# Kernel tuning notes

Hardware: AMD Instinct MI355X
Metric: run time of the kernel (lower is better)

The kernel has to match this reference:

```python
import jax, jax.numpy as jnp
import numpy as np

RES = 0.03
NUM_ROTS = 36
NUM_PROPOSAL = 256
OVERSAMPLE = 4           # fixed-size stand-in for the data-dependent while loop
GX, GY, GZ = 272, 112, 272  # grid covering [-4,4.16] x [-0.2,3.16] x [-4,4.16] at res=0.03
POW = 0.5
SEED_DIST_THRESH = 0.3


def setup_inputs() -> dict:
    key = jax.random.key(0)
    ks = jax.random.split(key, 6)
    N, M = 100000, 1024
    extent = jnp.array([7.0, 3.0, 7.0], jnp.float32)
    offset = jnp.array([-3.5, 0.0, -3.5], jnp.float32)
    pc = jax.random.uniform(ks[0], (N, 3), jnp.float32) * extent + offset
    xyz = jax.random.uniform(ks[1], (N, 3), jnp.float32, minval=-0.3, maxval=0.3)
    scale = jax.random.uniform(ks[2], (N, 3), jnp.float32, minval=0.1, maxval=1.0)
    prob = jax.random.uniform(ks[3], (N,), jnp.float32)
    corners = jnp.array([[-4.0, -0.2, -4.0], [4.16, 3.16, 4.16]], jnp.float32)
    vote_points = jax.random.uniform(ks[4], (M, 3), jnp.float32) * extent + offset
    return dict(pc=pc, xyz=xyz, scale=scale, prob=prob, corners=corners, vote_points=vote_points)


def hough_vote(pc, xyz, scale, prob, corners):
    # Each point casts NUM_ROTS votes: center = pc + R_y(theta) @ xyz_offset
    thetas = 2.0 * jnp.pi * jnp.arange(NUM_ROTS, dtype=jnp.float32) / NUM_ROTS
    c, s = jnp.cos(thetas), jnp.sin(thetas)  # [R]
    ox, oy, oz = xyz[:, 0:1], xyz[:, 1:2], xyz[:, 2:3]  # [N,1]
    rx = ox * c + oz * s      # [N,R]
    rz = -ox * s + oz * c     # [N,R]
    tx = pc[:, 0:1] + rx
    ty = jnp.broadcast_to(pc[:, 1:2] + oy, tx.shape)
    tz = pc[:, 2:3] + rz
    ix = jnp.floor((tx - corners[0, 0]) / RES + 0.5).astype(jnp.int32)
    iy = jnp.floor((ty - corners[0, 1]) / RES + 0.5).astype(jnp.int32)
    iz = jnp.floor((tz - corners[0, 2]) / RES + 0.5).astype(jnp.int32)
    inb = ((ix >= 0) & (ix < GX) & (iy >= 0) & (iy < GY) & (iz >= 0) & (iz < GZ))
    ixc = jnp.clip(ix, 0, GX - 1)
    iyc = jnp.clip(iy, 0, GY - 1)
    izc = jnp.clip(iz, 0, GZ - 1)
    flat = ((ixc * GY + iyc) * GZ + izc).ravel()  # [N*R]
    w = (prob[:, None] * inb.astype(prob.dtype))  # [N,R]
    grid_obj = jnp.zeros((GX * GY * GZ,), pc.dtype).at[flat].add(w.ravel())
    ws = (w[:, :, None] * scale[:, None, :]).reshape(-1, 3)
    grid_scale = jnp.zeros((GX * GY * GZ, 3), pc.dtype).at[flat].add(ws)
    hv_map = grid_obj.reshape(GX, GY, GZ)
    hv_scale = (grid_scale / (grid_obj[:, None] + 1e-7)).reshape(GX, GY, GZ, 3)
    return hv_map, hv_scale


def reference(pc, xyz, scale, prob, corners, vote_points):
    hv_map, hv_scale = hough_vote(pc, xyz, scale, prob, corners)
    hv_map_y = jnp.power(hv_map.max(axis=1) + 1e-7, POW)  # [GX,GZ]
    hv_map_yidx = jnp.argmax(hv_map, axis=1)              # [GX,GZ]
    dist = hv_map_y.reshape(-1)
    finite = jnp.isfinite(dist)
    safe = jnp.where(finite, dist, 0.0)
    ok = finite.all() & (safe.sum() >= 1e-7)
    dist = jnp.where(ok, safe, 1.0)

    # fixed-size oversampling instead of the data-dependent while loop
    K = NUM_PROPOSAL * OVERSAMPLE
    sample = jax.random.categorical(jax.random.key(42), jnp.log(dist + 1e-30), shape=(K,))
    sample_val = dist[sample]
    xi = sample // GZ
    zi = sample % GZ
    yi = hv_map_yidx[xi, zi]
    world_loc = jnp.stack([xi, yi, zi], -1).astype(pc.dtype) * RES + corners[0]  # [K,3]
    sc = hv_scale[xi, yi, zi, :]  # [K,3]

    # min distance to vote seeds; keep candidates near seeds (fallback: keep all)
    d2seed = jnp.min(jnp.linalg.norm(world_loc[:, None, :] - vote_points[None, :, :], axis=-1), axis=-1)
    keep = d2seed < SEED_DIST_THRESH
    keep = jnp.where(keep.any(), keep, jnp.ones_like(keep))
    order = jnp.argsort(jnp.where(keep, 0, 1))  # stable: passing candidates first
    sel = order[:NUM_PROPOSAL]
    candidates = world_loc[sel]
    scales_out = sc[sel]
    probs = jnp.zeros((NUM_PROPOSAL,), pc.dtype)
    return candidates, probs, scales_out
```

## Files before the change

### kernel.cpp

```cpp
#include <hip/hip_runtime.h>
#include <math.h>
#include <stdio.h>
#include <stdint.h>

#define GXD 272
#define GYD 112
#define GZD 272
#define NROT 36
#define CCLS (GXD*GZD)
#define KSMP 1024
#define NPROP 256
#define HSLOTS 2048
#define YH 56
#define NBINS (GXD*2)
#define SLICE (GYD*GZD)
#define SVCAP 64
#define ROWG 16

struct RotTab { float c[NROT]; float s[NROT]; };

__device__ __forceinline__ uint32_t cell_hash(int flat) {
    return ((uint32_t)flat * 2654435761u) >> 21;
}

#define ROTL_AB(x, r) __builtin_amdgcn_alignbit((x), (x), 32u - (r))

__device__ __forceinline__ void threefry2x32(uint32_t k0, uint32_t k1,
                                             uint32_t x0, uint32_t x1,
                                             uint32_t& o0, uint32_t& o1) {
    uint32_t ks2 = k0 ^ k1 ^ 0x1BD11BDAu;
#define TF_ROUND(r) { x0 += x1; x1 = ROTL_AB(x1, r); x1 ^= x0; }
    x0 += k0; x1 += k1;
    TF_ROUND(13) TF_ROUND(15) TF_ROUND(26) TF_ROUND(6)
    x0 += k1;  x1 += ks2 + 1u;
    TF_ROUND(17) TF_ROUND(29) TF_ROUND(16) TF_ROUND(24)
    x0 += ks2; x1 += k0 + 2u;
    TF_ROUND(13) TF_ROUND(15) TF_ROUND(26) TF_ROUND(6)
    x0 += k0;  x1 += k1 + 3u;
    TF_ROUND(17) TF_ROUND(29) TF_ROUND(16) TF_ROUND(24)
    x0 += k1;  x1 += ks2 + 4u;
    TF_ROUND(13) TF_ROUND(15) TF_ROUND(26) TF_ROUND(6)
    x0 += ks2; x1 += k0 + 5u;
#undef TF_ROUND
    o0 = x0; o1 = x1;
}

__device__ __forceinline__ uint32_t tf_bits(uint32_t i) {
    uint32_t o0, o1;
    threefry2x32(0u, 42u, 0u, i, o0, o1);
    return o0 ^ o1;
}

__device__ __forceinline__ float uniform_from_bits(uint32_t b) {
    const float TINY = 1.1754943508222875e-38f;
    float f = __uint_as_float((b >> 9) | 0x3f800000u) - 1.0f;
    float u = __fadd_rn(__fmul_rn(f, 1.0f), TINY);
    return fmaxf(TINY, u);
}

__device__ __forceinline__ float gumbel_from_u(float u) {
    float l1 = (float)log((double)u);
    float l2 = (float)log((double)(-l1));
    return -l2;
}

__device__ __forceinline__ bool vote_iy(float py, float oy, float c0y, int& iy) {
    float ty = __fadd_rn(py, oy);
    float vy = __fadd_rn(__fdiv_rn(__fsub_rn(ty, c0y), 0.03f), 0.5f);
    iy = (int)floorf(vy);
    return (iy >= 0 && iy < GYD);
}
__device__ __forceinline__ bool vote_xz(float px, float pz, float ox, float oz,
                                        float c, float s, float c0x, float c0z,
                                        int& ix, int& iz) {
    float rx = __fadd_rn(__fmul_rn(ox, c), __fmul_rn(oz, s));
    float rz = __fadd_rn(__fmul_rn(-ox, s), __fmul_rn(oz, c));
    float tx = __fadd_rn(px, rx);
    float tz = __fadd_rn(pz, rz);
    float vx = __fadd_rn(__fdiv_rn(__fsub_rn(tx, c0x), 0.03f), 0.5f);
    float vz = __fadd_rn(__fdiv_rn(__fsub_rn(tz, c0z), 0.03f), 0.5f);
    ix = (int)floorf(vx);
    iz = (int)floorf(vz);
    return (ix >= 0 && ix < GXD && iz >= 0 && iz < GZD);
}
__device__ __forceinline__ bool vote_cell(float px, float py, float pz,
                                          float ox, float oy, float oz,
                                          float c, float s,
                                          float c0x, float c0y, float c0z,
                                          int& flat) {
    int iy, ix, iz;
    if (!vote_iy(py, oy, c0y, iy)) return false;
    if (!vote_xz(px, pz, ox, oz, c, s, c0x, c0z, ix, iz)) return false;
    flat = (ix*GYD + iy)*GZD + iz;
    return true;
}

__global__ __launch_bounds__(256) void k_count(const float* __restrict__ pc, const float* __restrict__ xyz,
                          const float* __restrict__ corners, int N, RotTab rt,
                          int* __restrict__ bincnt) {
    __shared__ int h[NBINS];
    int tid = threadIdx.x;
    for (int j = tid; j < NBINS; j += 256) h[j] = 0;
    __syncthreads();
    int i = blockIdx.x * 256 + tid;
    if (i < N) {
        float px = pc[3*i], py = pc[3*i+1], pz = pc[3*i+2];
        float ox = xyz[3*i], oy = xyz[3*i+1], oz = xyz[3*i+2];
        int iy;
        if (vote_iy(py, oy, corners[1], iy)) {
            int ybit = (iy >= YH) ? 1 : 0;
            float c0x = corners[0], c0z = corners[2];
            for (int r = 0; r < NROT; ++r) {
                int ix, iz;
                if (vote_xz(px, pz, ox, oz, rt.c[r], rt.s[r], c0x, c0z, ix, iz))
                    atomicAdd(&h[ix*2 + ybit], 1);
            }
        }
    }
    __syncthreads();
    for (int j = tid; j < NBINS; j += 256) if (h[j]) atomicAdd(&bincnt[j], h[j]);
}

__global__ __launch_bounds__(576) void k_prefix(const int* __restrict__ bincnt,
                         int* __restrict__ binbase, int* __restrict__ bincur) {
    __shared__ int sc[576];
    int tid = threadIdx.x;
    int v = (tid < NBINS) ? bincnt[tid] : 0;
    sc[tid] = v;
    __syncthreads();
    for (int off = 1; off < 576; off <<= 1) {
        int x = sc[tid];
        if (tid >= off) x += sc[tid - off];
        __syncthreads();
        sc[tid] = x;
        __syncthreads();
    }
    if (tid < NBINS) {
        int excl = sc[tid] - v;
        binbase[tid] = excl;
        bincur[tid] = excl;
    }
}

__global__ __launch_bounds__(256) void k_binwrite(const float* __restrict__ pc, const float* __restrict__ xyz,
                          const float* __restrict__ prob, const float* __restrict__ corners,
                          int N, RotTab rt, int* __restrict__ bincur,
                          int* __restrict__ vflat, float* __restrict__ vw) {
    __shared__ int h[NBINS];
    __shared__ int bbase[NBINS];
    int tid = threadIdx.x;
    for (int j = tid; j < NBINS; j += 256) h[j] = 0;
    __syncthreads();
    int i = blockIdx.x * 256 + tid;
    float px=0, py=0, pz=0, ox=0, oy=0, oz=0, w0=0, c0x=0, c0z=0;
    int iy = -1, ybit = 0;
    bool act = false;
    if (i < N) {
        px = pc[3*i]; py = pc[3*i+1]; pz = pc[3*i+2];
        ox = xyz[3*i]; oy = xyz[3*i+1]; oz = xyz[3*i+2];
        w0 = prob[i];
        c0x = corners[0]; c0z = corners[2];
        if (vote_iy(py, oy, corners[1], iy)) {
            act = true;
            ybit = (iy >= YH) ? 1 : 0;
        }
    }
    if (act) {
        for (int r = 0; r < NROT; ++r) {
            int ix, iz;
            if (vote_xz(px, pz, ox, oz, rt.c[r], rt.s[r], c0x, c0z, ix, iz))
                atomicAdd(&h[ix*2 + ybit], 1);
        }
    }
    __syncthreads();
    for (int j = tid; j < NBINS; j += 256) {
        int cnt = h[j];
        bbase[j] = cnt ? atomicAdd(&bincur[j], cnt) : 0;
        h[j] = 0;
    }
    __syncthreads();
    if (act) {
        for (int r = 0; r < NROT; ++r) {
            int ix, iz;
            if (vote_xz(px, pz, ox, oz, rt.c[r], rt.s[r], c0x, c0z, ix, iz)) {
                int bin = ix*2 + ybit;
                int rank = atomicAdd(&h[bin], 1);
                int slot = bbase[bin] + rank;
                vflat[slot] = (ix*GYD + iy)*GZD + iz;
                vw[slot] = w0;
            }
        }
    }
}

__global__ __launch_bounds__(256) void k_accum(const int* __restrict__ binbase,
                          const int* __restrict__ bincnt,
                          const int* __restrict__ vflat, const float* __restrict__ vw,
                          float* __restrict__ gobj) {
    __shared__ float tile[YH*GZD];
    int b = blockIdx.x;
    int x = b >> 1, yh = b & 1;
    int tid = threadIdx.x;
    for (int j = tid; j < YH*GZD; j += 256) tile[j] = 0.0f;
    __syncthreads();
    int lo = binbase[b], n = bincnt[b];
    int xoff = x * SLICE;
    int yoff = yh * (YH*GZD);
    for (int j = lo + tid; j < lo + n; j += 256) {
        int rel = vflat[j] - xoff;
        atomicAdd(&tile[rel - yoff], vw[j]);
    }
    __syncthreads();
    float* dst = gobj + (size_t)xoff + yoff;
    for (int j = tid; j < YH*GZD; j += 256) dst[j] = tile[j];
}

__global__ __launch_bounds__(256) void k_colmax(const float* __restrict__ gobj,
                         float* __restrict__ logits, int* __restrict__ yidx,
                         float* __restrict__ sumdist) {
    int c = blockIdx.x * blockDim.x + threadIdx.x;
    float d = 0.0f;
    if (c < CCLS) {
        int x = c / GZD, z = c % GZD;
        const float* base = gobj + (size_t)x*GYD*GZD + z;
        float m = base[0];
        int mi = 0;
        for (int y = 1; y < GYD; ++y) {
            float v = base[(size_t)y*GZD];
            if (v > m) { m = v; mi = y; }
        }
        d = __fsqrt_rn(__fadd_rn(m, 1e-7f));
        yidx[c] = mi;
        logits[c] = (float)log((double)__fadd_rn(d, 1e-30f));
    }
    __shared__ float sred[256];
    int tid = threadIdx.x;
    sred[tid] = d; __syncthreads();
    for (int off = 128; off > 0; off >>= 1) {
        if (tid < off) sred[tid] += sred[tid+off];
        __syncthreads();
    }
    if (tid == 0) atomicAdd(sumdist, sred[0]);
}

__global__ __launch_bounds__(256) void k_thresh(const float* __restrict__ logits,
                                                const float* __restrict__ sumdist,
                                                uint32_t* __restrict__ bth) {
    int c = blockIdx.x * blockDim.x + threadIdx.x;
    if (c >= CCLS) return;
    double B0 = log((double)*sumdist) - 3.0;
    double t = exp(-exp((double)logits[c] - (B0 - 0.05)));
    long long k_th = (long long)floor(t * 8388608.0) - 2;
    uint32_t b;
    if (k_th <= 0)              b = 0u;
    else if (k_th >= 8388608LL) b = 0xFFFFFFFFu;
    else                        b = (uint32_t)k_th << 9;
    bth[c] = b;
}

__global__ __launch_bounds__(256) void k_prefilter(const uint32_t* __restrict__ bth,
                                                   int* __restrict__ svcnt,
                                                   uint2* __restrict__ svrec) {
    int c = blockIdx.x * 256 + threadIdx.x;
    int k0 = blockIdx.y * (KSMP / ROWG);
    uint32_t th = bth[c];
    uint32_t i = (uint32_t)k0 * (uint32_t)CCLS + (uint32_t)c;
#pragma unroll 4
    for (int kk = 0; kk < KSMP / ROWG; ++kk) {
        uint32_t bits = tf_bits(i);
        if (__builtin_expect(bits >= th, 0)) {
            int row = k0 + kk;
            int idx = atomicAdd(&svcnt[row], 1);
            if (idx < SVCAP) svrec[row * SVCAP + idx] = make_uint2((uint32_t)c, bits);
        }
        i += (uint32_t)CCLS;
    }
}

__global__ __launch_bounds__(256) void k_finalize(const float* __restrict__ logits,
                                                  const int* __restrict__ svcnt,
                                                  const uint2* __restrict__ svrec,
                                                  int* __restrict__ samples) {
    int k = blockIdx.x;
    int tid = threadIdx.x;
    int n = svcnt[k];
    float best = -INFINITY; int bc = 0x7fffffff;
    if (n > 0 && n <= SVCAP) {
        if (tid < n) {
            uint2 rec = svrec[k * SVCAP + tid];
            int c = (int)rec.x;
            best = __fadd_rn(gumbel_from_u(uniform_from_bits(rec.y)), logits[c]);
            bc = c;
        }
    } else {
        uint32_t base = (uint32_t)k * (uint32_t)CCLS;
        for (int c = tid; c < CCLS; c += 256) {
            float v = __fadd_rn(gumbel_from_u(uniform_from_bits(tf_bits(base + (uint32_t)c))), logits[c]);
            if (v > best || (v == best && c < bc)) { best = v; bc = c; }
        }
    }
    __shared__ float sv[256];
    __shared__ int   si[256];
    sv[tid] = best; si[tid] = bc; __syncthreads();
    for (int off = 128; off > 0; off >>= 1) {
        if (tid < off) {
            float v2 = sv[tid+off]; int i2 = si[tid+off];
            if (v2 > sv[tid] || (v2 == sv[tid] && i2 < si[tid])) { sv[tid] = v2; si[tid] = i2; }
        }
        __syncthreads();
    }
    if (tid == 0) samples[k] = si[0];
}

__global__ __launch_bounds__(256) void k_build_table(const int* __restrict__ samples,
                                                     const int* __restrict__ yidx,
                                                     int* __restrict__ hkeys,
                                                     float* __restrict__ gsmall) {
    int tid = threadIdx.x;
    for (int j = tid; j < HSLOTS; j += 256) hkeys[j] = -1;
    for (int j = tid; j < 3*HSLOTS; j += 256) gsmall[j] = 0.0f;
    __syncthreads();
    for (int k = tid; k < KSMP; k += 256) {
        int s = samples[k];
        int xi = s / GZD, zi = s % GZD;
        int yi = yidx[s];
        int flat = (xi*GYD + yi)*GZD + zi;
        uint32_t h = cell_hash(flat);
        for (;;) {
            int prev = atomicCAS(&hkeys[h], -1, flat);
            if (prev == -1 || prev == flat) break;
            h = (h + 1) & (HSLOTS - 1);
        }
    }
}

__global__ __launch_bounds__(256) void k_scale_scatter(const float* __restrict__ pc, const float* __restrict__ xyz,
                          const float* __restrict__ scale, const float* __restrict__ prob,
                          const float* __restrict__ corners,
                          const int* __restrict__ hkeys, float* __restrict__ gsmall,
                          int N, RotTab rt) {
    __shared__ int lk[HSLOTS];
    for (int j = threadIdx.x; j < HSLOTS; j += 256) lk[j] = hkeys[j];
    __syncthreads();
    int i = blockIdx.x * blockDim.x + threadIdx.x;
    int r = blockIdx.y;
    if (i >= N) return;
    int flat;
    if (!vote_cell(pc[3*i], pc[3*i+1], pc[3*i+2], xyz[3*i], xyz[3*i+1], xyz[3*i+2],
                   rt.c[r], rt.s[r], corners[0], corners[1], corners[2], flat)) return;
    uint32_t h = cell_hash(flat);
    int slot = -1;
    for (;;) {
        int key = lk[h];
        if (key == flat) { slot = (int)h; break; }
        if (key == -1) break;
        h = (h + 1) & (HSLOTS - 1);
    }
    if (slot < 0) return;
    float w0 = prob[i];
    atomicAdd(&gsmall[3*slot+0], __fmul_rn(w0, scale[3*i]));
    atomicAdd(&gsmall[3*slot+1], __fmul_rn(w0, scale[3*i+1]));
    atomicAdd(&gsmall[3*slot+2], __fmul_rn(w0, scale[3*i+2]));
}

__global__ __launch_bounds__(256) void k_post(const float* __restrict__ gobj,
                       const int* __restrict__ hkeys, const float* __restrict__ gsmall,
                       const int* __restrict__ yidx, const int* __restrict__ samples,
                       const float* __restrict__ corners, const float* __restrict__ vp, int M,
                       float* __restrict__ world, float* __restrict__ scv, int* __restrict__ keep) {
    int k = blockIdx.x;
    int tid = threadIdx.x;
    int s = samples[k];
    int xi = s / GZD, zi = s % GZD;
    int yi = yidx[s];
    float wx = __fadd_rn(__fmul_rn((float)xi, 0.03f), corners[0]);
    float wy = __fadd_rn(__fmul_rn((float)yi, 0.03f), corners[1]);
    float wz = __fadd_rn(__fmul_rn((float)zi, 0.03f), corners[2]);

    float dmin = INFINITY;
    for (int j = tid; j < M; j += 256) {
        float dx = __fsub_rn(wx, vp[3*j]);
        float dy = __fsub_rn(wy, vp[3*j+1]);
        float dz = __fsub_rn(wz, vp[3*j+2]);
        float sq = __fadd_rn(__fadd_rn(__fmul_rn(dx,dx), __fmul_rn(dy,dy)), __fmul_rn(dz,dz));
        dmin = fminf(dmin, __fsqrt_rn(sq));
    }
    __shared__ float sm[256];
    sm[tid] = dmin; __syncthreads();
    for (int off = 128; off > 0; off >>= 1) {
        if (tid < off) sm[tid] = fminf(sm[tid], sm[tid+off]);
        __syncthreads();
    }
    if (tid == 0) {
        world[3*k] = wx; world[3*k+1] = wy; world[3*k+2] = wz;
        int flat = (xi*GYD + yi)*GZD + zi;
        uint32_t h = cell_hash(flat);
        while (hkeys[h] != flat) h = (h + 1) & (HSLOTS - 1);
        float go = __fadd_rn(gobj[flat], 1e-7f);
        scv[3*k+0] = __fdiv_rn(gsmall[3*h+0], go);
        scv[3*k+1] = __fdiv_rn(gsmall[3*h+1], go);
        scv[3*k+2] = __fdiv_rn(gsmall[3*h+2], go);
        keep[k] = (sm[0] < 0.3f) ? 1 : 0;
    }
}

__global__ __launch_bounds__(256) void k_select(const float* __restrict__ world,
                                                const float* __restrict__ scv,
                                                const int* __restrict__ keep,
                                                float* __restrict__ out) {
    __shared__ int kp[KSMP];
    __shared__ int tsum[256];
    __shared__ int sel[NPROP];
    __shared__ int anyk;
    int tid = threadIdx.x;
    if (tid == 0) anyk = 0;
    __syncthreads();
    int a = 0;
    for (int j = tid; j < KSMP; j += 256) { int v = keep[j]; kp[j] = v; a |= v; }
    if (a) anyk = 1;
    __syncthreads();
    int any = anyk;
    int j0 = tid * 4;
    int k0v = any ? kp[j0]   : 1;
    int k1v = any ? kp[j0+1] : 1;
    int k2v = any ? kp[j0+2] : 1;
    int k3v = any ? kp[j0+3] : 1;
    int s0 = k0v, s1 = s0 + k1v, s2 = s1 + k2v, s3 = s2 + k3v;
    tsum[tid] = s3;
    __syncthreads();
    for (int off = 1; off < 256; off <<= 1) {
        int x = tsum[tid];
        if (tid >= off) x += tsum[tid - off];
        __syncthreads();
        tsum[tid] = x;
        __syncthreads();
    }
    int base = (tid > 0) ? tsum[tid-1] : 0;
    int nk = tsum[255];
    int inc[4] = { base + s0, base + s1, base + s2, base + s3 };
    int kv[4]  = { k0v, k1v, k2v, k3v };
    for (int q = 0; q < 4; ++q) {
        int j = j0 + q;
        int slot = kv[q] ? (inc[q] - 1) : (nk + j - inc[q]);
        if (slot < NPROP) sel[slot] = j;
    }
    __syncthreads();
    if (tid < NPROP) {
        int sidx = sel[tid];
        out[3*tid+0] = world[3*sidx+0];
        out[3*tid+1] = world[3*sidx+1];
        out[3*tid+2] = world[3*sidx+2];
        out[3*NPROP + tid] = 0.0f;
        out[4*NPROP + 3*tid + 0] = scv[3*sidx+0];
        out[4*NPROP + 3*tid + 1] = scv[3*sidx+1];
        out[4*NPROP + 3*tid + 2] = scv[3*sidx+2];
    }
}

extern "C" void kernel_launch(void* const* d_in, const int* in_sizes, int n_in,
                              void* d_out, int out_size, void* d_ws, size_t ws_size,
                              hipStream_t stream) {
    const float* pc      = (const float*)d_in[0];
    const float* xyz     = (const float*)d_in[1];
    const float* scale   = (const float*)d_in[2];
    const float* prob    = (const float*)d_in[3];
    const float* corners = (const float*)d_in[4];
    const float* vp      = (const float*)d_in[5];
    int N = in_sizes[0] / 3;
    int M = in_sizes[5] / 3;
    int NV = N * NROT;

    const size_t G = (size_t)GXD * GYD * GZD;
    float* gobj    = (float*)d_ws;
    float* sumdist = gobj + G;
    int*   bincnt  = (int*)(sumdist + 1);
    int*   svcnt   = bincnt + NBINS;
    int*   binbase = svcnt + KSMP;
    int*   bincur  = binbase + NBINS;
    float* logits  = (float*)(bincur + NBINS);
    uint32_t* bth  = (uint32_t*)(logits + CCLS);
    int*   yidx    = (int*)(bth + CCLS);
    int*   samples = yidx + CCLS;
    int*   hkeys   = samples + KSMP;
    float* gsmall  = (float*)(hkeys + HSLOTS);
    float* world   = gsmall + 3*HSLOTS;
    float* scv     = world + 3*KSMP;
    int*   keep    = (int*)(scv + 3*KSMP);
    uint2* svrec   = (uint2*)(((uintptr_t)(keep + KSMP) + 15) & ~(uintptr_t)15);
    int*   vflat   = (int*)(svrec + (size_t)KSMP * SVCAP);
    float* vw      = (float*)(vflat + NV);
    size_t need = (size_t)((char*)(vw + NV) - (char*)d_ws);
    if (ws_size < need) {
        fprintf(stderr, "kernel_launch: ws_size %zu < needed %zu\n", ws_size, need);
        return;
    }

    hipMemsetAsync(sumdist, 0, (1 + NBINS + KSMP)*sizeof(int), stream);

    RotTab rt;
    const float twopi = (float)(2.0 * M_PI);
    for (int r = 0; r < NROT; ++r) {
        float th = (twopi * (float)r) / 36.0f;
        rt.c[r] = (float)cos((double)th);
        rt.s[r] = (float)sin((double)th);
    }

    int pblocks = (N + 255) / 256;
    k_count<<<pblocks, 256, 0, stream>>>(pc, xyz, corners, N, rt, bincnt);
    k_prefix<<<1, 576, 0, stream>>>(bincnt, binbase, bincur);
    k_binwrite<<<pblocks, 256, 0, stream>>>(pc, xyz, prob, corners, N, rt, bincur, vflat, vw);
    k_accum<<<NBINS, 256, 0, stream>>>(binbase, bincnt, vflat, vw, gobj);
    k_colmax<<<(CCLS + 255) / 256, 256, 0, stream>>>(gobj, logits, yidx, sumdist);
    k_thresh<<<(CCLS + 255) / 256, 256, 0, stream>>>(logits, sumdist, bth);
    dim3 pf_grid(CCLS / 256, ROWG);
    k_prefilter<<<pf_grid, 256, 0, stream>>>(bth, svcnt, svrec);
    k_finalize<<<KSMP, 256, 0, stream>>>(logits, svcnt, svrec, samples);
    k_build_table<<<1, 256, 0, stream>>>(samples, yidx, hkeys, gsmall);
    dim3 sgrid(pblocks, NROT);
    k_scale_scatter<<<sgrid, 256, 0, stream>>>(pc, xyz, scale, prob, corners, hkeys, gsmall, N, rt);
    k_post<<<KSMP, 256, 0, stream>>>(gobj, hkeys, gsmall, yidx, samples, corners, vp, M, world, scv, keep);
    k_select<<<1, 256, 0, stream>>>(world, scv, keep, (float*)d_out);
}
```

Baseline: 422.7 us.

## Replace count+prefix passes with per-block segment arena binning; loop rotations in scale scatter

Removes the separate counting and global prefix kernels. Each binwrite block now reserves one contiguous arena range with a single atomic and records a per-bin segment (start, count). The accumulate kernel rebuilds each bin's element list by scanning its segments and binary-searching the prefix. The scale scatter kernel now loops over the 36 rotations inside each thread instead of using a 2D grid, so per-point loads and the y test are done once. The costs are extra scan and binary-search work in accumulate, scattered segment reads, and a hard cap of 512 blocks per bin.

```diff
diff --git a/kernel.cpp b/kernel.cpp
--- a/kernel.cpp
+++ b/kernel.cpp
@@ -16,6 +16,7 @@
 #define SLICE (GYD*GZD)
 #define SVCAP 64
 #define ROWG 16
+#define MAXSEG 512
 
 struct RotTab { float c[NROT]; float s[NROT]; };
 
@@ -83,74 +84,21 @@
     iz = (int)floorf(vz);
     return (ix >= 0 && ix < GXD && iz >= 0 && iz < GZD);
 }
-__device__ __forceinline__ bool vote_cell(float px, float py, float pz,
-                                          float ox, float oy, float oz,
-                                          float c, float s,
-                                          float c0x, float c0y, float c0z,
-                                          int& flat) {
-    int iy, ix, iz;
-    if (!vote_iy(py, oy, c0y, iy)) return false;
-    if (!vote_xz(px, pz, ox, oz, c, s, c0x, c0z, ix, iz)) return false;
-    flat = (ix*GYD + iy)*GZD + iz;
-    return true;
-}
-
-__global__ __launch_bounds__(256) void k_count(const float* __restrict__ pc, const float* __restrict__ xyz,
-                          const float* __restrict__ corners, int N, RotTab rt,
-                          int* __restrict__ bincnt) {
-    __shared__ int h[NBINS];
-    int tid = threadIdx.x;
-    for (int j = tid; j < NBINS; j += 256) h[j] = 0;
-    __syncthreads();
-    int i = blockIdx.x * 256 + tid;
-    if (i < N) {
-        float px = pc[3*i], py = pc[3*i+1], pz = pc[3*i+2];
-        float ox = xyz[3*i], oy = xyz[3*i+1], oz = xyz[3*i+2];
-        int iy;
-        if (vote_iy(py, oy, corners[1], iy)) {
-            int ybit = (iy >= YH) ? 1 : 0;
-            float c0x = corners[0], c0z = corners[2];
-            for (int r = 0; r < NROT; ++r) {
-                int ix, iz;
-                if (vote_xz(px, pz, ox, oz, rt.c[r], rt.s[r], c0x, c0z, ix, iz))
-                    atomicAdd(&h[ix*2 + ybit], 1);
-            }
-        }
-    }
-    __syncthreads();
-    for (int j = tid; j < NBINS; j += 256) if (h[j]) atomicAdd(&bincnt[j], h[j]);
-}
-
-__global__ __launch_bounds__(576) void k_prefix(const int* __restrict__ bincnt,
-                         int* __restrict__ binbase, int* __restrict__ bincur) {
-    __shared__ int sc[576];
-    int tid = threadIdx.x;
-    int v = (tid < NBINS) ? bincnt[tid] : 0;
-    sc[tid] = v;
-    __syncthreads();
-    for (int off = 1; off < 576; off <<= 1) {
-        int x = sc[tid];
-        if (tid >= off) x += sc[tid - off];
-        __syncthreads();
-        sc[tid] = x;
-        __syncthreads();
-    }
-    if (tid < NBINS) {
-        int excl = sc[tid] - v;
-        binbase[tid] = excl;
-        bincur[tid] = excl;
-    }
-}
 
 __global__ __launch_bounds__(256) void k_binwrite(const float* __restrict__ pc, const float* __restrict__ xyz,
                           const float* __restrict__ prob, const float* __restrict__ corners,
-                          int N, RotTab rt, int* __restrict__ bincur,
+                          int N, RotTab rt,
+                          int* __restrict__ arena_cur, int* __restrict__ segcnt,
+                          int2* __restrict__ segrec,
                           int* __restrict__ vflat, float* __restrict__ vw) {
     __shared__ int h[NBINS];
-    __shared__ int bbase[NBINS];
+    __shared__ int loff[NBINS];
+    __shared__ int tsum[256];
+    __shared__ int sbase;
     int tid = threadIdx.x;
     for (int j = tid; j < NBINS; j += 256) h[j] = 0;
     __syncthreads();
+
     int i = blockIdx.x * 256 + tid;
     float px=0, py=0, pz=0, ox=0, oy=0, oz=0, w0=0, c0x=0, c0z=0;
     int iy = -1, ybit = 0;
@@ -173,19 +121,45 @@
         }
     }
     __syncthreads();
+
+    int c0 = h[tid];
+    int c1 = h[tid + 256];
+    int c2 = (tid < NBINS - 512) ? h[tid + 512] : 0;
+    tsum[tid] = c0 + c1 + c2;
+    __syncthreads();
+    for (int off = 1; off < 256; off <<= 1) {
+        int v = tsum[tid];
+        if (tid >= off) v += tsum[tid - off];
+        __syncthreads();
+        tsum[tid] = v;
+        __syncthreads();
+    }
+    int base = (tid > 0) ? tsum[tid-1] : 0;
+    int total = tsum[255];
+    if (tid == 0) sbase = total ? atomicAdd(arena_cur, total) : 0;
+    loff[tid] = base;
+    loff[tid + 256] = base + c0;
+    if (tid < NBINS - 512) loff[tid + 512] = base + c0 + c1;
+    __syncthreads();
+    int gb = sbase;
+
     for (int j = tid; j < NBINS; j += 256) {
         int cnt = h[j];
-        bbase[j] = cnt ? atomicAdd(&bincur[j], cnt) : 0;
+        if (cnt) {
+            int idx = atomicAdd(&segcnt[j], 1);
+            if (idx < MAXSEG) segrec[j*MAXSEG + idx] = make_int2(gb + loff[j], cnt);
+        }
         h[j] = 0;
     }
     __syncthreads();
+
     if (act) {
         for (int r = 0; r < NROT; ++r) {
             int ix, iz;
             if (vote_xz(px, pz, ox, oz, rt.c[r], rt.s[r], c0x, c0z, ix, iz)) {
                 int bin = ix*2 + ybit;
                 int rank = atomicAdd(&h[bin], 1);
-                int slot = bbase[bin] + rank;
+                int slot = gb + loff[bin] + rank;
                 vflat[slot] = (ix*GYD + iy)*GZD + iz;
                 vw[slot] = w0;
             }
@@ -193,22 +167,50 @@
     }
 }
 
-__global__ __launch_bounds__(256) void k_accum(const int* __restrict__ binbase,
-                          const int* __restrict__ bincnt,
+__global__ __launch_bounds__(256) void k_accum(const int* __restrict__ segcnt,
+                          const int2* __restrict__ segrec,
                           const int* __restrict__ vflat, const float* __restrict__ vw,
                           float* __restrict__ gobj) {
     __shared__ float tile[YH*GZD];
+    __shared__ int sstart[512];
+    __shared__ int spre[513];
     int b = blockIdx.x;
     int x = b >> 1, yh = b & 1;
     int tid = threadIdx.x;
     for (int j = tid; j < YH*GZD; j += 256) tile[j] = 0.0f;
-    __syncthreads();
-    int lo = binbase[b], n = bincnt[b];
+    int ns = segcnt[b];
+    int a0 = 0, a1 = 0, st0 = 0, st1 = 0;
+    if (tid < ns)       { int2 r = segrec[b*MAXSEG + tid];       st0 = r.x; a0 = r.y; }
+    if (tid + 256 < ns) { int2 r = segrec[b*MAXSEG + tid + 256]; st1 = r.x; a1 = r.y; }
+    sstart[tid] = a0 + a1;
+    __syncthreads();
+    for (int off = 1; off < 256; off <<= 1) {
+        int v = sstart[tid];
+        if (tid >= off) v += sstart[tid - off];
+        __syncthreads();
+        sstart[tid] = v;
+        __syncthreads();
+    }
+    int base = (tid > 0) ? sstart[tid-1] : 0;
+    int total = sstart[255];
+    __syncthreads();
+    spre[2*tid]   = base;
+    spre[2*tid+1] = base + a0;
+    sstart[2*tid]   = st0;
+    sstart[2*tid+1] = st1;
+    if (tid == 0) spre[512] = total;
+    __syncthreads();
     int xoff = x * SLICE;
     int yoff = yh * (YH*GZD);
-    for (int j = lo + tid; j < lo + n; j += 256) {
-        int rel = vflat[j] - xoff;
-        atomicAdd(&tile[rel - yoff], vw[j]);
+    for (int t = tid; t < total; t += 256) {
+        int lo = 0, hi = 511;
+        while (lo < hi) {
+            int mid = (lo + hi + 1) >> 1;
+            if (spre[mid] <= t) lo = mid; else hi = mid - 1;
+        }
+        int idx = sstart[lo] + (t - spre[lo]);
+        int rel = vflat[idx] - xoff - yoff;
+        atomicAdd(&tile[rel], vw[idx]);
     }
     __syncthreads();
     float* dst = gobj + (size_t)xoff + yoff;
@@ -342,25 +344,34 @@
     __shared__ int lk[HSLOTS];
     for (int j = threadIdx.x; j < HSLOTS; j += 256) lk[j] = hkeys[j];
     __syncthreads();
-    int i = blockIdx.x * blockDim.x + threadIdx.x;
-    int r = blockIdx.y;
+    int i = blockIdx.x * 256 + threadIdx.x;
     if (i >= N) return;
-    int flat;
-    if (!vote_cell(pc[3*i], pc[3*i+1], pc[3*i+2], xyz[3*i], xyz[3*i+1], xyz[3*i+2],
-                   rt.c[r], rt.s[r], corners[0], corners[1], corners[2], flat)) return;
-    uint32_t h = cell_hash(flat);
-    int slot = -1;
-    for (;;) {
-        int key = lk[h];
-        if (key == flat) { slot = (int)h; break; }
-        if (key == -1) break;
-        h = (h + 1) & (HSLOTS - 1);
-    }
-    if (slot < 0) return;
+    float px = pc[3*i], py = pc[3*i+1], pz = pc[3*i+2];
+    float ox = xyz[3*i], oy = xyz[3*i+1], oz = xyz[3*i+2];
+    float c0x = corners[0], c0z = corners[2];
+    int iy;
+    if (!vote_iy(py, oy, corners[1], iy)) return;
     float w0 = prob[i];
-    atomicAdd(&gsmall[3*slot+0], __fmul_rn(w0, scale[3*i]));
-    atomicAdd(&gsmall[3*slot+1], __fmul_rn(w0, scale[3*i+1]));
-    atomicAdd(&gsmall[3*slot+2], __fmul_rn(w0, scale[3*i+2]));
+    float wsx = __fmul_rn(w0, scale[3*i]);
+    float wsy = __fmul_rn(w0, scale[3*i+1]);
+    float wsz = __fmul_rn(w0, scale[3*i+2]);
+    for (int r = 0; r < NROT; ++r) {
+        int ix, iz;
+        if (!vote_xz(px, pz, ox, oz, rt.c[r], rt.s[r], c0x, c0z, ix, iz)) continue;
+        int flat = (ix*GYD + iy)*GZD + iz;
+        uint32_t h = cell_hash(flat);
+        int slot = -1;
+        for (;;) {
+            int key = lk[h];
+            if (key == flat) { slot = (int)h; break; }
+            if (key == -1) break;
+            h = (h + 1) & (HSLOTS - 1);
+        }
+        if (slot < 0) continue;
+        atomicAdd(&gsmall[3*slot+0], wsx);
+        atomicAdd(&gsmall[3*slot+1], wsy);
+        atomicAdd(&gsmall[3*slot+2], wsz);
+    }
 }
 
 __global__ __launch_bounds__(256) void k_post(const float* __restrict__ gobj,
@@ -469,33 +480,35 @@
     int N = in_sizes[0] / 3;
     int M = in_sizes[5] / 3;
     int NV = N * NROT;
+    int pblocks = (N + 255) / 256;
 
     const size_t G = (size_t)GXD * GYD * GZD;
-    float* gobj    = (float*)d_ws;
-    float* sumdist = gobj + G;
-    int*   bincnt  = (int*)(sumdist + 1);
-    int*   svcnt   = bincnt + NBINS;
-    int*   binbase = svcnt + KSMP;
-    int*   bincur  = binbase + NBINS;
-    float* logits  = (float*)(bincur + NBINS);
-    uint32_t* bth  = (uint32_t*)(logits + CCLS);
-    int*   yidx    = (int*)(bth + CCLS);
-    int*   samples = yidx + CCLS;
-    int*   hkeys   = samples + KSMP;
-    float* gsmall  = (float*)(hkeys + HSLOTS);
-    float* world   = gsmall + 3*HSLOTS;
-    float* scv     = world + 3*KSMP;
-    int*   keep    = (int*)(scv + 3*KSMP);
-    uint2* svrec   = (uint2*)(((uintptr_t)(keep + KSMP) + 15) & ~(uintptr_t)15);
-    int*   vflat   = (int*)(svrec + (size_t)KSMP * SVCAP);
-    float* vw      = (float*)(vflat + NV);
+    float* gobj      = (float*)d_ws;
+    float* sumdist   = gobj + G;
+    int*   svcnt     = (int*)(sumdist + 1);
+    int*   segcnt    = svcnt + KSMP;
+    int*   arena_cur = segcnt + NBINS;
+    float* logits    = (float*)(arena_cur + 1);
+    uint32_t* bth    = (uint32_t*)(logits + CCLS);
+    int*   yidx      = (int*)(bth + CCLS);
+    int*   samples   = yidx + CCLS;
+    int*   hkeys     = samples + KSMP;
+    float* gsmall    = (float*)(hkeys + HSLOTS);
+    float* world     = gsmall + 3*HSLOTS;
+    float* scv       = world + 3*KSMP;
+    int*   keep      = (int*)(scv + 3*KSMP);
+    uint2* svrec     = (uint2*)(((uintptr_t)(keep + KSMP) + 15) & ~(uintptr_t)15);
+    int2*  segrec    = (int2*)(svrec + (size_t)KSMP * SVCAP);
+    int*   vflat     = (int*)(segrec + (size_t)NBINS * MAXSEG);
+    float* vw        = (float*)(vflat + NV);
     size_t need = (size_t)((char*)(vw + NV) - (char*)d_ws);
-    if (ws_size < need) {
-        fprintf(stderr, "kernel_launch: ws_size %zu < needed %zu\n", ws_size, need);
+    if (ws_size < need || pblocks > MAXSEG) {
+        fprintf(stderr, "kernel_launch: ws %zu < need %zu or pblocks %d > %d\n",
+                ws_size, need, pblocks, MAXSEG);
         return;
     }
 
-    hipMemsetAsync(sumdist, 0, (1 + NBINS + KSMP)*sizeof(int), stream);
+    hipMemsetAsync(sumdist, 0, (1 + KSMP + NBINS + 1)*sizeof(int), stream);
 
     RotTab rt;
     const float twopi = (float)(2.0 * M_PI);
@@ -505,19 +518,16 @@
         rt.s[r] = (float)sin((double)th);
     }
 
-    int pblocks = (N + 255) / 256;
-    k_count<<<pblocks, 256, 0, stream>>>(pc, xyz, corners, N, rt, bincnt);
-    k_prefix<<<1, 576, 0, stream>>>(bincnt, binbase, bincur);
-    k_binwrite<<<pblocks, 256, 0, stream>>>(pc, xyz, prob, corners, N, rt, bincur, vflat, vw);
-    k_accum<<<NBINS, 256, 0, stream>>>(binbase, bincnt, vflat, vw, gobj);
+    k_binwrite<<<pblocks, 256, 0, stream>>>(pc, xyz, prob, corners, N, rt,
+                                            arena_cur, segcnt, segrec, vflat, vw);
+    k_accum<<<NBINS, 256, 0, stream>>>(segcnt, segrec, vflat, vw, gobj);
     k_colmax<<<(CCLS + 255) / 256, 256, 0, stream>>>(gobj, logits, yidx, sumdist);
     k_thresh<<<(CCLS + 255) / 256, 256, 0, stream>>>(logits, sumdist, bth);
     dim3 pf_grid(CCLS / 256, ROWG);
     k_prefilter<<<pf_grid, 256, 0, stream>>>(bth, svcnt, svrec);
     k_finalize<<<KSMP, 256, 0, stream>>>(logits, svcnt, svrec, samples);
     k_build_table<<<1, 256, 0, stream>>>(samples, yidx, hkeys, gsmall);
-    dim3 sgrid(pblocks, NROT);
-    k_scale_scatter<<<sgrid, 256, 0, stream>>>(pc, xyz, scale, prob, corners, hkeys, gsmall, N, rt);
+    k_scale_scatter<<<pblocks, 256, 0, stream>>>(pc, xyz, scale, prob, corners, hkeys, gsmall, N, rt);
     k_post<<<KSMP, 256, 0, stream>>>(gobj, hkeys, gsmall, yidx, samples, corners, vp, M, world, scv, keep);
     k_select<<<1, 256, 0, stream>>>(world, scv, keep, (float*)d_out);
 }
```

After: 440.8 us. 1.04x slower.
